# Optimization experiments

Measured on AMD Instinct MI355X. Metric: run time of the kernel, lower is better.

## Reference

```python
import jax, jax.numpy as jnp
import numpy as np

DIM = 768
HEADS = 12

def setup_inputs() -> dict:
    key = jax.random.key(0)
    ks = jax.random.split(key, 5)
    x = jax.random.normal(ks[0], (8, 1024, DIM), dtype=jnp.float32)
    s = 1.0 / np.sqrt(DIM)
    W_qkv = jax.random.normal(ks[1], (DIM, 3 * DIM), dtype=jnp.float32) * s
    b_qkv = jax.random.normal(ks[2], (3 * DIM,), dtype=jnp.float32) * 0.01
    W_proj = jax.random.normal(ks[3], (DIM, DIM), dtype=jnp.float32) * s
    b_proj = jax.random.normal(ks[4], (DIM,), dtype=jnp.float32) * 0.01
    return {"x": x, "W_qkv": W_qkv, "b_qkv": b_qkv, "W_proj": W_proj, "b_proj": b_proj}

def reference(x, W_qkv, b_qkv, W_proj, b_proj):
    B, T, D = x.shape
    H = HEADS
    hd = D // H
    scale = hd ** -0.5
    qkv = x @ W_qkv + b_qkv                      # [B,T,3D]
    qkv = qkv.reshape(B, T, 3, H, hd)
    q, k, v = jnp.moveaxis(qkv, 2, 0)            # each [B,T,H,hd]
    q = jnp.transpose(q, (0, 2, 1, 3))           # [B,H,T,hd]
    k = jnp.transpose(k, (0, 2, 1, 3))
    v = jnp.transpose(v, (0, 2, 1, 3))
    attn = jnp.einsum('bhqd,bhkd->bhqk', q, k) * scale
    attn = jax.nn.softmax(attn, axis=-1)
    y = jnp.einsum('bhqk,bhkd->bhqd', attn, v)   # [B,H,T,hd]
    y = jnp.transpose(y, (0, 2, 1, 3)).reshape(B, T, D)
    return y @ W_proj + b_proj
```

## Files before the change

### kernel.cpp

```cpp
#include <hip/hip_runtime.h>

typedef unsigned short u16;
typedef __attribute__((ext_vector_type(8))) short short8;
typedef __attribute__((ext_vector_type(4))) short short4v;
typedef __attribute__((ext_vector_type(2))) int int2v;
typedef __attribute__((ext_vector_type(4))) float f32x4;

#define DIM   768
#define HEADS 12
#define HD    64
#define BATCH 8
#define SEQ   1024
#define MTOK  (BATCH*SEQ)
#define NQKV  (3*DIM)
#define KP    72
#define EPAD  66
#define PSZ   ((size_t)BATCH*HEADS*SEQ*HD)
#define SCQ   0.1803368801f

__device__ __forceinline__ u16 f2bf(float f) {
  unsigned x = __float_as_uint(f);
  x += 0x7fffu + ((x >> 16) & 1u);
  return (u16)(x >> 16);
}

__device__ __forceinline__ void gload16(const u16* g, u16* l) {
  __builtin_amdgcn_global_load_lds(
      (const __attribute__((address_space(1))) unsigned int*)g,
      (__attribute__((address_space(3))) unsigned int*)l, 16, 0, 0);
}

#define XBLK 6144
#define QTBLK 1728
__global__ void cvt_all_k(const float* __restrict__ x,
                          const float* __restrict__ Wqkv,
                          const float* __restrict__ Wproj,
                          u16* __restrict__ xb, u16* __restrict__ wqkvt,
                          u16* __restrict__ wprojt) {
  __shared__ u16 tile[32][33];
  const int blk = blockIdx.x;
  if (blk < XBLK) {
    const int i = blk * 256 + threadIdx.x;
    float4 f = ((const float4*)x)[i];
    short4v o;
    o.x = (short)f2bf(f.x); o.y = (short)f2bf(f.y);
    o.z = (short)f2bf(f.z); o.w = (short)f2bf(f.w);
    ((short4v*)xb)[i] = o;
    return;
  }
  const float* in; u16* out; int K, N, n0, k0;
  if (blk < XBLK + QTBLK) {
    const int t = blk - XBLK;
    in = Wqkv; out = wqkvt; K = DIM; N = NQKV;
    n0 = (t % (NQKV / 32)) * 32; k0 = (t / (NQKV / 32)) * 32;
  } else {
    const int t = blk - XBLK - QTBLK;
    in = Wproj; out = wprojt; K = DIM; N = DIM;
    n0 = (t % (DIM / 32)) * 32; k0 = (t / (DIM / 32)) * 32;
  }
  const int tx = threadIdx.x & 31, ty = threadIdx.x >> 5;
  #pragma unroll
  for (int i = 0; i < 32; i += 8)
    tile[ty + i][tx] = f2bf(in[(size_t)(k0 + ty + i) * N + n0 + tx]);
  __syncthreads();
  #pragma unroll
  for (int i = 0; i < 32; i += 8)
    out[(size_t)(n0 + ty + i) * K + k0 + tx] = tile[tx][ty + i];
}

__global__ __launch_bounds__(256)
void gemm_qkv(const u16* __restrict__ A, const u16* __restrict__ Bt,
              const float* __restrict__ bias, u16* __restrict__ qkv) {
  __shared__ __align__(16) u16 smem[8 * 128 * 32];
  const int w = threadIdx.x >> 6, lane = threadIdx.x & 63;
  const int l15 = lane & 15, quad = lane >> 4;
  const int b_ = blockIdx.x;
  const int xcd = b_ & 7, j = b_ >> 3;
  const int m0 = ((j & 7) * 8 + xcd) * 128;
  const int n0 = (j >> 3) * 128;
  const int wm = (w >> 1) * 64, wn = (w & 1) * 64;

  f32x4 acc[4][4] = {};

  const int ar = threadIdx.x >> 2, ak = (threadIdx.x & 3) * 8;
  const u16* ga = A  + (size_t)(m0 + ar) * DIM + ak;
  const u16* gb = Bt + (size_t)(n0 + ar) * DIM + ak;
  const int lo = threadIdx.x * 8;

  auto qstage = [&](int c, int k0) {
    u16* base = smem + c * 16384;
    #pragma unroll
    for (int t = 0; t < 2; ++t) {
      gload16(ga + (size_t)t * 64 * DIM + k0,      base + lo + t * 2048);
      gload16(ga + (size_t)t * 64 * DIM + k0 + 32, base + 4096  + lo + t * 2048);
      gload16(gb + (size_t)t * 64 * DIM + k0,      base + 8192  + lo + t * 2048);
      gload16(gb + (size_t)t * 64 * DIM + k0 + 32, base + 12288 + lo + t * 2048);
    }
  };

  qstage(0, 0);

  #pragma unroll
  for (int it = 0; it < 12; ++it) {
    const int cur = it & 1;
    if (it < 11) qstage(cur ^ 1, (it + 1) * 64);
    if (it < 11) asm volatile("s_waitcnt vmcnt(8)" ::: "memory");
    else         asm volatile("s_waitcnt vmcnt(0)" ::: "memory");
    __builtin_amdgcn_s_barrier();

    const u16* hb = smem + cur * 16384;
    short8 af[4][2], bfr[4][2];
    #pragma unroll
    for (int kh = 0; kh < 2; ++kh) {
      const u16* lAh = hb + kh * 4096;
      const u16* lBh = hb + 8192 + kh * 4096;
      #pragma unroll
      for (int mt = 0; mt < 4; ++mt)
        af[mt][kh] = *(const short8*)&lAh[(wm + mt * 16 + l15) * 32 + quad * 8];
      #pragma unroll
      for (int nt = 0; nt < 4; ++nt)
        bfr[nt][kh] = *(const short8*)&lBh[(wn + nt * 16 + l15) * 32 + quad * 8];
    }

    asm volatile("s_waitcnt lgkmcnt(0)" ::: "memory");
    __builtin_amdgcn_s_barrier();

    #pragma unroll
    for (int kh = 0; kh < 2; ++kh)
      #pragma unroll
      for (int mt = 0; mt < 4; ++mt)
        #pragma unroll
        for (int nt = 0; nt < 4; ++nt)
          acc[mt][nt] = __builtin_amdgcn_mfma_f32_16x16x32_bf16(af[mt][kh], bfr[nt][kh], acc[mt][nt], 0, 0, 0);
  }

  const int bb = m0 >> 10;
  const int tb0 = (m0 & 1023) + wm;
  const int nh = n0 + wn;
  const int part = nh / DIM, idx = nh - part * DIM;
  const int h = idx >> 6;

  float bnl[4];
  #pragma unroll
  for (int nt = 0; nt < 4; ++nt) bnl[nt] = bias[nh + nt * 16 + l15];

  if (part < 2) {
    u16* dstbase = qkv + part * PSZ + ((size_t)(bb * HEADS + h) * SEQ + tb0) * HD;
    const float qsc = (part == 0) ? SCQ : 1.0f;
    const int erow = lane >> 3, ec8 = (lane & 7) * 8;
    #pragma unroll
    for (int mt = 0; mt < 4; ++mt) {
      u16* ep = smem + w * (16 * EPAD) + (mt & 1) * (4 * 16 * EPAD);
      #pragma unroll
      for (int nt = 0; nt < 4; ++nt)
        #pragma unroll
        for (int r = 0; r < 4; ++r)
          ep[(quad * 4 + r) * EPAD + nt * 16 + l15] = f2bf((acc[mt][nt][r] + bnl[nt]) * qsc);
      #pragma unroll
      for (int j2 = 0; j2 < 2; ++j2) {
        const int trow = j2 * 8 + erow;
        short8 vrow = *(const short8*)&ep[trow * EPAD + ec8];
        *(short8*)(dstbase + (size_t)(mt * 16 + trow) * HD + ec8) = vrow;
      }
    }
  } else {
    u16* vrow0 = qkv + 2 * PSZ + (size_t)(bb * HEADS + h) * HD * SEQ;
    #pragma unroll
    for (int nt = 0; nt < 4; ++nt) {
      const int d = nt * 16 + l15;
      u16* trow = vrow0 + (size_t)d * SEQ + tb0 + quad * 4;
      #pragma unroll
      for (int mt = 0; mt < 4; ++mt) {
        short4v pv;
        pv.x = (short)f2bf(acc[mt][nt][0] + bnl[nt]);
        pv.y = (short)f2bf(acc[mt][nt][1] + bnl[nt]);
        pv.z = (short)f2bf(acc[mt][nt][2] + bnl[nt]);
        pv.w = (short)f2bf(acc[mt][nt][3] + bnl[nt]);
        *(short4v*)(trow + mt * 16) = pv;
      }
    }
  }
}

__global__ __launch_bounds__(256)
void gemm_proj(const u16* __restrict__ A, const u16* __restrict__ Bt,
               const float* __restrict__ bias, float* __restrict__ outF) {
  __shared__ __align__(16) u16 smem[8 * 128 * 32];
  const int w = threadIdx.x >> 6, lane = threadIdx.x & 63;
  const int l15 = lane & 15, quad = lane >> 4;
  const int b_ = blockIdx.x;
  const int xcd = b_ & 7, j = b_ >> 3;
  const int m0 = ((j & 7) * 8 + xcd) * 128;
  const int n0 = (j >> 3) * 128;
  const int wm = (w >> 1) * 64, wn = (w & 1) * 64;

  f32x4 acc[4][4] = {};

  const int ar = threadIdx.x >> 2, ak = (threadIdx.x & 3) * 8;
  const u16* ga = A  + (size_t)(m0 + ar) * DIM + ak;
  const u16* gb = Bt + (size_t)(n0 + ar) * DIM + ak;
  const int lo = threadIdx.x * 8;

  auto pstage = [&](int c, int k0) {
    u16* base = smem + c * 16384;
    #pragma unroll
    for (int t = 0; t < 2; ++t) {
      gload16(ga + (size_t)t * 64 * DIM + k0,      base + lo + t * 2048);
      gload16(ga + (size_t)t * 64 * DIM + k0 + 32, base + 4096  + lo + t * 2048);
      gload16(gb + (size_t)t * 64 * DIM + k0,      base + 8192  + lo + t * 2048);
      gload16(gb + (size_t)t * 64 * DIM + k0 + 32, base + 12288 + lo + t * 2048);
    }
  };

  pstage(0, 0);
  __syncthreads();

  #pragma unroll
  for (int it = 0; it < 12; ++it) {
    const int cur = it & 1;
    if (it < 11) pstage(cur ^ 1, (it + 1) * 64);
    const u16* hb = smem + cur * 16384;
    #pragma unroll
    for (int kh = 0; kh < 2; ++kh) {
      const u16* lAh = hb + kh * 4096;
      const u16* lBh = hb + 8192 + kh * 4096;
      short8 af[4], bfr[4];
      #pragma unroll
      for (int mt = 0; mt < 4; ++mt)
        af[mt] = *(const short8*)&lAh[(wm + mt * 16 + l15) * 32 + quad * 8];
      #pragma unroll
      for (int nt = 0; nt < 4; ++nt)
        bfr[nt] = *(const short8*)&lBh[(wn + nt * 16 + l15) * 32 + quad * 8];
      #pragma unroll
      for (int mt = 0; mt < 4; ++mt)
        #pragma unroll
        for (int nt = 0; nt < 4; ++nt)
          acc[mt][nt] = __builtin_amdgcn_mfma_f32_16x16x32_bf16(af[mt], bfr[nt], acc[mt][nt], 0, 0, 0);
    }
    __syncthreads();
  }

  #pragma unroll
  for (int nt = 0; nt < 4; ++nt) {
    const int n = n0 + wn + nt * 16 + l15;
    const float bn = bias[n];
    #pragma unroll
    for (int mt = 0; mt < 4; ++mt)
      #pragma unroll
      for (int r = 0; r < 4; ++r) {
        const int m = m0 + wm + mt * 16 + quad * 4 + r;
        outF[(size_t)m * DIM + n] = acc[mt][nt][r] + bn;
      }
  }
}

__global__ __launch_bounds__(512, 4)
void attn_k(const u16* __restrict__ qb, const u16* __restrict__ kb,
            const u16* __restrict__ vtb, u16* __restrict__ yb) {
  const int bh = blockIdx.x, qt = blockIdx.y;
  const int tid = threadIdx.x;
  const int w = tid >> 6, lane = tid & 63;
  const int l15 = lane & 15, quad = lane >> 4;
  const int rg = w & 3;
  const int kh = w >> 2;
  const int nt0 = kh * 2;

  __shared__ __align__(16) u16 smem[26624];
  u16* lPq = smem + 16384 + rg * 2304;
  u16* stg = smem + 17408 + rg * 2304;
  float* fo = (float*)smem;

  const u16* qrow = qb + ((size_t)bh * SEQ + qt * 128 + rg * 32 + l15) * HD;
  short8 aq[2][2];
  #pragma unroll
  for (int qg = 0; qg < 2; ++qg) {
    aq[qg][0] = *(const short8*)(qrow + (size_t)qg * 16 * HD + quad * 8);
    aq[qg][1] = *(const short8*)(qrow + (size_t)qg * 16 * HD + 32 + quad * 8);
  }

  f32x4 o[2][4] = {};
  f32x4 sum[2] = {};

  const u16* kcbase = kb + (size_t)bh * SEQ * HD;
  const u16* vbase  = vtb + (size_t)bh * HD * SEQ;

  const int srow = tid >> 3;
  const int schunk = (tid & 7) ^ (srow & 7);
  const u16* kgs = kcbase + (size_t)srow * HD + schunk * 8;
  const u16* vgs = vbase + (size_t)srow * SEQ + schunk * 8;
  const int dst = tid * 8;

  auto stage = [&](int c, int kc) {
    gload16(kgs + kc * 4096, smem + c * 8192 + dst);
    gload16(vgs + kc * 64,   smem + c * 8192 + 4096 + dst);
  };

  short8 ones;
  #pragma unroll
  for (int i = 0; i < 8; ++i) ones[i] = (short)0x3f80;

  stage(0, 0);

  for (int kc = 0; kc < 16; ++kc) {
    const int cur = kc & 1;
    if (kc < 15) stage(cur ^ 1, kc + 1);
    if (kc < 15) asm volatile("s_waitcnt vmcnt(2)" ::: "memory");
    else         asm volatile("s_waitcnt vmcnt(0)" ::: "memory");
    __builtin_amdgcn_s_barrier();

    const u16* lK = smem + cur * 8192;
    const u16* lV = lK + 4096;
    const int sx = l15 & 7;

    short8 akf[2][2];
    #pragma unroll
    for (int i = 0; i < 2; ++i) {
      const int key = (nt0 + i) * 16 + l15;
      akf[i][0] = *(const short8*)&lK[key * 64 + ((quad ^ sx) * 8)];
      akf[i][1] = *(const short8*)&lK[key * 64 + (((4 + quad) ^ sx) * 8)];
    }

    #pragma unroll
    for (int qg = 0; qg < 2; ++qg) {
      f32x4 s0 = {}, s1 = {};
      __builtin_amdgcn_s_setprio(1);
      s0 = __builtin_amdgcn_mfma_f32_16x16x32_bf16(akf[0][0], aq[qg][0], s0, 0, 0, 0);
      s0 = __builtin_amdgcn_mfma_f32_16x16x32_bf16(akf[0][1], aq[qg][1], s0, 0, 0, 0);
      s1 = __builtin_amdgcn_mfma_f32_16x16x32_bf16(akf[1][0], aq[qg][0], s1, 0, 0, 0);
      s1 = __builtin_amdgcn_mfma_f32_16x16x32_bf16(akf[1][1], aq[qg][1], s1, 0, 0, 0);
      __builtin_amdgcn_s_setprio(0);
      #pragma unroll
      for (int i = 0; i < 2; ++i) {
        const f32x4 s = i ? s1 : s0;
        float p0 = __builtin_amdgcn_exp2f(s[0]);
        float p1 = __builtin_amdgcn_exp2f(s[1]);
        float p2 = __builtin_amdgcn_exp2f(s[2]);
        float p3 = __builtin_amdgcn_exp2f(s[3]);
        int2v pkk;
        pkk.x = (int)__builtin_amdgcn_perm(__float_as_uint(p1), __float_as_uint(p0), 0x07060302u);
        pkk.y = (int)__builtin_amdgcn_perm(__float_as_uint(p3), __float_as_uint(p2), 0x07060302u);
        *(int2v*)&lPq[(qg * 16 + l15) * KP + (nt0 + i) * 16 + quad * 4] = pkk;
      }
    }

    short8 bv[4];
    #pragma unroll
    for (int ntd = 0; ntd < 4; ++ntd)
      bv[ntd] = *(const short8*)&lV[(ntd * 16 + l15) * 64 + (((kh * 4 + quad) ^ sx) * 8)];

    #pragma unroll
    for (int qg = 0; qg < 2; ++qg) {
      const short8 ap = *(const short8*)&lPq[(qg * 16 + l15) * KP + kh * 32 + quad * 8];
      __builtin_amdgcn_s_setprio(1);
      #pragma unroll
      for (int ntd = 0; ntd < 4; ++ntd)
        o[qg][ntd] = __builtin_amdgcn_mfma_f32_16x16x32_bf16(ap, bv[ntd], o[qg][ntd], 0, 0, 0);
      sum[qg] = __builtin_amdgcn_mfma_f32_16x16x32_bf16(ap, ones, sum[qg], 0, 0, 0);
      __builtin_amdgcn_s_setprio(0);
    }

    asm volatile("s_waitcnt lgkmcnt(0)" ::: "memory");
    __builtin_amdgcn_s_barrier();
  }

  if (kh == 1) {
    #pragma unroll
    for (int qg = 0; qg < 2; ++qg)
      #pragma unroll
      for (int r = 0; r < 4; ++r) {
        const int row = rg * 32 + qg * 16 + quad * 4 + r;
        #pragma unroll
        for (int ntd = 0; ntd < 4; ++ntd)
          fo[row * 68 + ntd * 16 + l15] = o[qg][ntd][r];
        if (l15 == 0) fo[row * 68 + 64] = sum[qg][r];
      }
  }
  __syncthreads();

  if (kh == 0) {
    const int b = bh / HEADS, h = bh % HEADS;
    #pragma unroll
    for (int qg = 0; qg < 2; ++qg)
      #pragma unroll
      for (int r = 0; r < 4; ++r) {
        const int lrow = qg * 16 + quad * 4 + r;
        const int row = rg * 32 + lrow;
        const float s = sum[qg][r] + fo[row * 68 + 64];
        const float inv = 1.0f / s;
        #pragma unroll
        for (int ntd = 0; ntd < 4; ++ntd) {
          const float v = (o[qg][ntd][r] + fo[row * 68 + ntd * 16 + l15]) * inv;
          stg[lrow * KP + ntd * 16 + l15] = f2bf(v);
        }
      }
    u16* dst2 = yb + ((size_t)b * SEQ + qt * 128 + rg * 32) * DIM + h * HD;
    const int erow = lane >> 3, ec8 = (lane & 7) * 8;
    #pragma unroll
    for (int j = 0; j < 4; ++j) {
      const int trow = j * 8 + erow;
      short8 vrow = *(const short8*)&stg[trow * KP + ec8];
      *(short8*)(dst2 + (size_t)trow * DIM + ec8) = vrow;
    }
  }
}

extern "C" void kernel_launch(void* const* d_in, const int* in_sizes, int n_in,
                              void* d_out, int out_size, void* d_ws, size_t ws_size,
                              hipStream_t stream) {
  const float* x     = (const float*)d_in[0];
  const float* Wqkv  = (const float*)d_in[1];
  const float* bqkv  = (const float*)d_in[2];
  const float* Wproj = (const float*)d_in[3];
  const float* bproj = (const float*)d_in[4];
  float* out = (float*)d_out;

  u16* xb     = (u16*)d_ws;
  u16* wqkvt  = xb + (size_t)MTOK * DIM;
  u16* wprojt = wqkvt + (size_t)NQKV * DIM;
  u16* qkv_b  = wprojt + (size_t)DIM * DIM;
  u16* y_b    = qkv_b + 3 * PSZ;

  cvt_all_k<<<XBLK + QTBLK + (DIM / 32) * (DIM / 32), 256, 0, stream>>>(
      x, Wqkv, Wproj, xb, wqkvt, wprojt);

  gemm_qkv<<<1152, 256, 0, stream>>>(xb, wqkvt, bqkv, qkv_b);

  attn_k<<<dim3(BATCH * HEADS, SEQ / 128), 512, 0, stream>>>(
      qkv_b, qkv_b + PSZ, qkv_b + 2 * PSZ, y_b);

  gemm_proj<<<384, 256, 0, stream>>>(y_b, wprojt, bproj, out);
}
```

Baseline: 173.4 us.

## Enlarge QKV GEMM tiles to 256x256 with swizzled LDS and 512 threads

The QKV projection GEMM moves from 128x128 tiles on 256 threads to 256x256 tiles on 512 threads. Each stage now holds a full 64-wide K slice, stored in LDS with an XOR swizzle to avoid bank conflicts. MFMAs are issued right after each half's fragment loads instead of after all loads. The larger tiles reuse more data from LDS and global memory, but the grid shrinks to 288 blocks of 128 KB LDS each, which risks a poor wave tail on the GPU's CUs and lower occupancy.

```diff
diff --git a/kernel.cpp b/kernel.cpp
--- a/kernel.cpp
+++ b/kernel.cpp
@@ -68,33 +68,33 @@
     out[(size_t)(n0 + ty + i) * K + k0 + tx] = tile[tx][ty + i];
 }
 
-__global__ __launch_bounds__(256)
+__global__ __launch_bounds__(512, 2)
 void gemm_qkv(const u16* __restrict__ A, const u16* __restrict__ Bt,
               const float* __restrict__ bias, u16* __restrict__ qkv) {
-  __shared__ __align__(16) u16 smem[8 * 128 * 32];
-  const int w = threadIdx.x >> 6, lane = threadIdx.x & 63;
+  __shared__ __align__(16) u16 smem[2 * 32768];
+  const int tid = threadIdx.x;
+  const int w = tid >> 6, lane = tid & 63;
   const int l15 = lane & 15, quad = lane >> 4;
   const int b_ = blockIdx.x;
   const int xcd = b_ & 7, j = b_ >> 3;
-  const int m0 = ((j & 7) * 8 + xcd) * 128;
-  const int n0 = (j >> 3) * 128;
-  const int wm = (w >> 1) * 64, wn = (w & 1) * 64;
-
-  f32x4 acc[4][4] = {};
-
-  const int ar = threadIdx.x >> 2, ak = (threadIdx.x & 3) * 8;
-  const u16* ga = A  + (size_t)(m0 + ar) * DIM + ak;
-  const u16* gb = Bt + (size_t)(n0 + ar) * DIM + ak;
-  const int lo = threadIdx.x * 8;
+  const int m0 = ((j & 3) * 8 + xcd) * 256;
+  const int n0 = (j >> 2) * 256;
+  const int wm = (w >> 2) * 128, wn = (w & 3) * 64;
+
+  f32x4 acc[8][4] = {};
+
+  const int srow = tid >> 3;
+  const int schunk = (tid & 7) ^ (srow & 7);
+  const u16* ga = A  + (size_t)(m0 + srow) * DIM + schunk * 8;
+  const u16* gb = Bt + (size_t)(n0 + srow) * DIM + schunk * 8;
+  const int ldst = tid * 8;
 
   auto qstage = [&](int c, int k0) {
-    u16* base = smem + c * 16384;
-    #pragma unroll
-    for (int t = 0; t < 2; ++t) {
-      gload16(ga + (size_t)t * 64 * DIM + k0,      base + lo + t * 2048);
-      gload16(ga + (size_t)t * 64 * DIM + k0 + 32, base + 4096  + lo + t * 2048);
-      gload16(gb + (size_t)t * 64 * DIM + k0,      base + 8192  + lo + t * 2048);
-      gload16(gb + (size_t)t * 64 * DIM + k0 + 32, base + 12288 + lo + t * 2048);
+    u16* base = smem + c * 32768;
+    #pragma unroll
+    for (int t = 0; t < 4; ++t) {
+      gload16(ga + (size_t)t * 64 * DIM + k0, base + t * 4096 + ldst);
+      gload16(gb + (size_t)t * 64 * DIM + k0, base + 16384 + t * 4096 + ldst);
     }
   };
 
@@ -108,30 +108,27 @@
     else         asm volatile("s_waitcnt vmcnt(0)" ::: "memory");
     __builtin_amdgcn_s_barrier();
 
-    const u16* hb = smem + cur * 16384;
-    short8 af[4][2], bfr[4][2];
+    const u16* lA = smem + cur * 32768;
+    const u16* lB = lA + 16384;
+    const int sx = l15 & 7;
     #pragma unroll
     for (int kh = 0; kh < 2; ++kh) {
-      const u16* lAh = hb + kh * 4096;
-      const u16* lBh = hb + 8192 + kh * 4096;
-      #pragma unroll
-      for (int mt = 0; mt < 4; ++mt)
-        af[mt][kh] = *(const short8*)&lAh[(wm + mt * 16 + l15) * 32 + quad * 8];
+      short8 af[8], bfr[4];
+      #pragma unroll
+      for (int mt = 0; mt < 8; ++mt)
+        af[mt] = *(const short8*)&lA[(wm + mt * 16 + l15) * 64 + (((kh * 4 + quad) ^ sx) * 8)];
       #pragma unroll
       for (int nt = 0; nt < 4; ++nt)
-        bfr[nt][kh] = *(const short8*)&lBh[(wn + nt * 16 + l15) * 32 + quad * 8];
+        bfr[nt] = *(const short8*)&lB[(wn + nt * 16 + l15) * 64 + (((kh * 4 + quad) ^ sx) * 8)];
+      #pragma unroll
+      for (int mt = 0; mt < 8; ++mt)
+        #pragma unroll
+        for (int nt = 0; nt < 4; ++nt)
+          acc[mt][nt] = __builtin_amdgcn_mfma_f32_16x16x32_bf16(af[mt], bfr[nt], acc[mt][nt], 0, 0, 0);
     }
 
     asm volatile("s_waitcnt lgkmcnt(0)" ::: "memory");
     __builtin_amdgcn_s_barrier();
-
-    #pragma unroll
-    for (int kh = 0; kh < 2; ++kh)
-      #pragma unroll
-      for (int mt = 0; mt < 4; ++mt)
-        #pragma unroll
-        for (int nt = 0; nt < 4; ++nt)
-          acc[mt][nt] = __builtin_amdgcn_mfma_f32_16x16x32_bf16(af[mt][kh], bfr[nt][kh], acc[mt][nt], 0, 0, 0);
   }
 
   const int bb = m0 >> 10;
@@ -149,8 +146,8 @@
     const float qsc = (part == 0) ? SCQ : 1.0f;
     const int erow = lane >> 3, ec8 = (lane & 7) * 8;
     #pragma unroll
-    for (int mt = 0; mt < 4; ++mt) {
-      u16* ep = smem + w * (16 * EPAD) + (mt & 1) * (4 * 16 * EPAD);
+    for (int mt = 0; mt < 8; ++mt) {
+      u16* ep = smem + w * (16 * EPAD) + (mt & 1) * (8 * 16 * EPAD);
       #pragma unroll
       for (int nt = 0; nt < 4; ++nt)
         #pragma unroll
@@ -170,7 +167,7 @@
       const int d = nt * 16 + l15;
       u16* trow = vrow0 + (size_t)d * SEQ + tb0 + quad * 4;
       #pragma unroll
-      for (int mt = 0; mt < 4; ++mt) {
+      for (int mt = 0; mt < 8; ++mt) {
         short4v pv;
         pv.x = (short)f2bf(acc[mt][nt][0] + bnl[nt]);
         pv.y = (short)f2bf(acc[mt][nt][1] + bnl[nt]);
@@ -423,7 +420,7 @@
   cvt_all_k<<<XBLK + QTBLK + (DIM / 32) * (DIM / 32), 256, 0, stream>>>(
       x, Wqkv, Wproj, xb, wqkvt, wprojt);
 
-  gemm_qkv<<<1152, 256, 0, stream>>>(xb, wqkvt, bqkv, qkv_b);
+  gemm_qkv<<<288, 512, 0, stream>>>(xb, wqkvt, bqkv, qkv_b);
 
   attn_k<<<dim3(BATCH * HEADS, SEQ / 128), 512, 0, stream>>>(
       qkv_b, qkv_b + PSZ, qkv_b + 2 * PSZ, y_b);
```

Measured after the change: 189.9 us. 9.5% more time.
